# Kernel tuning notes

Measured on AMD Instinct MI355X. Metric: run time of the kernel, lower is better.

## Reference

```python
import jax, jax.numpy as jnp
import numpy as np
import math

NP_, NA_ = 100000, 50000          # paper / author node counts
E0, E1, E2 = 300000, 300000, 200000  # author->paper, paper->author, paper->paper
H, D = 4, 16
HID = H * D                       # 64
IN_DIM, OUT_DIM = 128, 64
L = 2                             # num_layers
EPS = 1e-5


def _lin(x, W, b):
    return x @ W + b


def _ln(x, g, b):
    m = jnp.mean(x, axis=-1, keepdims=True)
    v = jnp.mean((x - m) ** 2, axis=-1, keepdims=True)
    return (x - m) * jax.lax.rsqrt(v + EPS) * g + b


def _segment_softmax(a, seg, n):
    m = jax.ops.segment_max(a, seg, num_segments=n)
    a = jnp.exp(a - m[seg])
    s = jax.ops.segment_sum(a, seg, num_segments=n)
    return a / (s[seg] + 1e-16)


def _hgt_conv(h_p, h_a, ei_ap, ei_pa, ei_pp,
              W_kqv, b_kqv, W_krel, W_vrel, p_rel, W_hout, b_hout, skip):
    # per-node-type fused KQV projection (HeteroDictLinear)
    kqv_p = _lin(h_p, W_kqv[0], b_kqv[0])   # [NP, 3*HID]
    kqv_a = _lin(h_a, W_kqv[1], b_kqv[1])   # [NA, 3*HID]
    k_p, q_p, v_p = [t.reshape(-1, H, D) for t in jnp.split(kqv_p, 3, axis=1)]
    k_a, q_a, v_a = [t.reshape(-1, H, D) for t in jnp.split(kqv_a, 3, axis=1)]
    # destination (query) concat order: paper then author -> dst offsets {paper:0, author:NP}
    Q = jnp.concatenate([q_p, q_a], axis=0)                    # [NP+NA, H, D]
    # per-(edge_type, head) DxD relation transforms on source k/v (k_rel / v_rel)
    # src concat order follows edge types: et0 src=author, et1 src=paper, et2 src=paper
    Ks = jnp.concatenate([
        jnp.einsum('nhd,hde->nhe', k_a, W_krel[0]),
        jnp.einsum('nhd,hde->nhe', k_p, W_krel[1]),
        jnp.einsum('nhd,hde->nhe', k_p, W_krel[2]),
    ], axis=0)                                                 # [NA+2*NP, H, D]
    Vs = jnp.concatenate([
        jnp.einsum('nhd,hde->nhe', v_a, W_vrel[0]),
        jnp.einsum('nhd,hde->nhe', v_p, W_vrel[1]),
        jnp.einsum('nhd,hde->nhe', v_p, W_vrel[2]),
    ], axis=0)
    # bipartite global edge index (src offsets: 0, NA, NA+NP; dst offsets: paper 0, author NP)
    src = jnp.concatenate([ei_ap[0], ei_pa[0] + NA_, ei_pp[0] + NA_ + NP_])
    dst = jnp.concatenate([ei_ap[1], ei_pa[1] + NP_, ei_pp[1]])
    p = jnp.concatenate([
        jnp.broadcast_to(p_rel[0], (E0, H)),
        jnp.broadcast_to(p_rel[1], (E1, H)),
        jnp.broadcast_to(p_rel[2], (E2, H)),
    ], axis=0)                                                 # [E, H]
    # edge-wise attention: alpha = (q_i * k_j).sum(-1) * p_rel / sqrt(D), segment-softmax over dst
    alpha = jnp.einsum('ehd,ehd->eh', Q[dst], Ks[src]) * p / math.sqrt(D)
    alpha = _segment_softmax(alpha, dst, NP_ + NA_)
    out = jax.ops.segment_sum(Vs[src] * alpha[:, :, None], dst,
                              num_segments=NP_ + NA_)          # [NP+NA, H, D]
    out = out.reshape(-1, HID)
    g = jax.nn.gelu(out, approximate=False)
    o_p = _lin(g[:NP_], W_hout[0], b_hout[0])
    o_a = _lin(g[NP_:], W_hout[1], b_hout[1])
    a_p = jax.nn.sigmoid(skip[0])
    a_a = jax.nn.sigmoid(skip[1])
    return a_p * o_p + (1.0 - a_p) * h_p, a_a * o_a + (1.0 - a_a) * h_a


def _forward(x_paper, x_author, ei_ap, ei_pa, ei_pp,
             W_in, b_in, W_kqv, b_kqv, W_krel, W_vrel, p_rel,
             W_hout, b_hout, skip, ln_g, ln_b, W_out, b_out):
    h_p = _lin(x_paper, W_in[0], b_in[0])
    h_a = _lin(x_author, W_in[1], b_in[1])
    for l in range(L):
        h_p, h_a = _hgt_conv(h_p, h_a, ei_ap, ei_pa, ei_pp,
                             W_kqv[l], b_kqv[l], W_krel[l], W_vrel[l],
                             p_rel[l], W_hout[l], b_hout[l], skip[l])
        h_p = jax.nn.gelu(_ln(h_p, ln_g[l, 0], ln_b[l, 0]), approximate=False)
        h_a = jax.nn.gelu(_ln(h_a, ln_g[l, 1], ln_b[l, 1]), approximate=False)
        # dropout is identity at eval
    out_p = _lin(h_p, W_out[0], b_out[0])
    out_a = _lin(h_a, W_out[1], b_out[1])
    return jnp.concatenate([out_p, out_a], axis=0)  # [NP+NA, OUT_DIM]


def setup_inputs() -> dict:
    key = jax.random.key(0)
    ks = jax.random.split(key, 20)
    f32 = jnp.float32

    def nrm(k, shape, fan_in):
        return jax.random.normal(k, shape, dtype=f32) * (1.0 / math.sqrt(fan_in))

    inp = {}
    inp['x_paper'] = jax.random.normal(ks[0], (NP_, IN_DIM), dtype=f32)
    inp['x_author'] = jax.random.normal(ks[1], (NA_, IN_DIM), dtype=f32)
    inp['ei_ap'] = jnp.stack([jax.random.randint(ks[2], (E0,), 0, NA_),
                              jax.random.randint(ks[3], (E0,), 0, NP_)]).astype(jnp.int32)
    inp['ei_pa'] = jnp.stack([jax.random.randint(ks[4], (E1,), 0, NP_),
                              jax.random.randint(ks[5], (E1,), 0, NA_)]).astype(jnp.int32)
    inp['ei_pp'] = jnp.stack([jax.random.randint(ks[6], (E2,), 0, NP_),
                              jax.random.randint(ks[7], (E2,), 0, NP_)]).astype(jnp.int32)
    inp['W_in'] = nrm(ks[8], (2, IN_DIM, HID), IN_DIM)
    inp['b_in'] = jnp.zeros((2, HID), f32)
    inp['W_kqv'] = nrm(ks[9], (L, 2, HID, 3 * HID), HID)
    inp['b_kqv'] = jnp.zeros((L, 2, 3 * HID), f32)
    inp['W_krel'] = nrm(ks[10], (L, 3, H, D, D), D)
    inp['W_vrel'] = nrm(ks[11], (L, 3, H, D, D), D)
    inp['p_rel'] = jnp.ones((L, 3, H), f32)
    inp['W_hout'] = nrm(ks[12], (L, 2, HID, HID), HID)
    inp['b_hout'] = jnp.zeros((L, 2, HID), f32)
    inp['skip'] = jnp.ones((L, 2), f32)
    inp['ln_g'] = jnp.ones((L, 2, HID), f32)
    inp['ln_b'] = jnp.zeros((L, 2, HID), f32)
    inp['W_out'] = nrm(ks[13], (2, HID, OUT_DIM), HID)
    inp['b_out'] = jnp.zeros((2, OUT_DIM), f32)
    return inp


def reference(x_paper, x_author, ei_ap, ei_pa, ei_pp,
              W_in, b_in, W_kqv, b_kqv, W_krel, W_vrel, p_rel,
              W_hout, b_hout, skip, ln_g, ln_b, W_out, b_out):
    return _forward(x_paper, x_author, ei_ap, ei_pa, ei_pp,
                    W_in, b_in, W_kqv, b_kqv, W_krel, W_vrel, p_rel,
                    W_hout, b_hout, skip, ln_g, ln_b, W_out, b_out)
```

## Files before the change

### kernel.cpp

```cpp
#include <hip/hip_runtime.h>
#include <hip/hip_bf16.h>

#define NP 100000
#define NA 50000
#define NTOT 150000
#define E0 300000
#define E1 300000
#define E2 200000
#define ETOT 800000
#define NH 4
#define HD 16
#define HID 64
#define IN_DIM 128
#define KQV 192
#define LAYERS 2
#define NSRC 250000
#define JP 320
#define JA 192
#define NCH 586
#define PT 1563
#define AT 782

typedef __attribute__((ext_vector_type(8))) short bf16x8;
typedef __attribute__((ext_vector_type(4))) float f32x4;
typedef _Float16 h16x2 __attribute__((ext_vector_type(2)));

__device__ __forceinline__ float gelu_exact(float x) {
    return 0.5f * x * (1.0f + erff(x * 0.7071067811865475f));
}
__device__ __forceinline__ unsigned short f2bf(float f) {
    unsigned u = __float_as_uint(f);
    return (unsigned short)((u + 0x7fffu + ((u >> 16) & 1u)) >> 16);
}
__device__ __forceinline__ float bf2f(unsigned short b) {
    return __uint_as_float((unsigned)b << 16);
}
__device__ __forceinline__ unsigned short f2h(float f) {
    union { _Float16 h; unsigned short u; } c;
    c.h = (_Float16)f;
    return c.u;
}

__device__ __forceinline__ void edge_decode(int e, const int* __restrict__ ei_ap,
                                            const int* __restrict__ ei_pa,
                                            const int* __restrict__ ei_pp,
                                            int& src, int& dst) {
    if (e < E0)            { src = ei_ap[e];                 dst = ei_ap[E0 + e]; }
    else if (e < E0 + E1)  { int le = e - E0;
                             src = NA + ei_pa[le];           dst = NP + ei_pa[E1 + le]; }
    else                   { int le = e - E0 - E1;
                             src = NA + NP + ei_pp[le];      dst = ei_pp[E2 + le]; }
}

__global__ void zero_int_kernel(int* __restrict__ p, int n) {
    int i = blockIdx.x * blockDim.x + threadIdx.x;
    int st = gridDim.x * blockDim.x;
    for (int j = i; j < n; j += st) p[j] = 0;
}

__global__ void csr_count_kernel(const int* __restrict__ ei_ap, const int* __restrict__ ei_pa,
                                 const int* __restrict__ ei_pp, int* __restrict__ cnt) {
    int e = blockIdx.x * 256 + threadIdx.x;
    if (e >= ETOT) return;
    int src, dst; edge_decode(e, ei_ap, ei_pa, ei_pp, src, dst);
    atomicAdd(&cnt[dst], 1);
}

__global__ void scan_chunk_sums(const int* __restrict__ cnt, int* __restrict__ csum) {
    __shared__ int sd[256];
    int c = blockIdx.x, t = threadIdx.x;
    int i = c * 256 + t;
    sd[t] = (i < NTOT) ? cnt[i] : 0;
    __syncthreads();
    for (int o = 128; o > 0; o >>= 1) { if (t < o) sd[t] += sd[t + o]; __syncthreads(); }
    if (t == 0) csum[c] = sd[0];
}

__global__ void scan_offsets(const int* __restrict__ csum, int* __restrict__ coff, int nch) {
    __shared__ int sd[1024];
    int t = threadIdx.x;
    int v = (t < nch) ? csum[t] : 0;
    sd[t] = v;
    __syncthreads();
    for (int o = 1; o < 1024; o <<= 1) {
        int x = (t >= o) ? sd[t - o] : 0;
        __syncthreads();
        sd[t] += x;
        __syncthreads();
    }
    if (t < nch) coff[t] = sd[t] - v;
}

__global__ void scan_final(const int* __restrict__ cnt, const int* __restrict__ coff,
                           int* __restrict__ row_ptr, int* __restrict__ cursor) {
    __shared__ int sd[256];
    int c = blockIdx.x, t = threadIdx.x, i = c * 256 + t;
    int v = (i < NTOT) ? cnt[i] : 0;
    sd[t] = v;
    __syncthreads();
    for (int o = 1; o < 256; o <<= 1) {
        int x = (t >= o) ? sd[t - o] : 0;
        __syncthreads();
        sd[t] += x;
        __syncthreads();
    }
    if (i < NTOT) { int ex = coff[c] + sd[t] - v; row_ptr[i] = ex; cursor[i] = ex; }
    if (i == 0) row_ptr[NTOT] = ETOT;
}

__global__ void csr_fill_kernel(const int* __restrict__ ei_ap, const int* __restrict__ ei_pa,
                                const int* __restrict__ ei_pp, int* __restrict__ cursor,
                                int* __restrict__ edge_src) {
    int e = blockIdx.x * 256 + threadIdx.x;
    if (e >= ETOT) return;
    int src, dst; edge_decode(e, ei_ap, ei_pa, ei_pp, src, dst);
    int pos = atomicAdd(&cursor[dst], 1);
    edge_src[pos] = src;
}

__global__ void fuse_weights_kernel(const float* __restrict__ Wkqv, const float* __restrict__ bkqv,
                                    const float* __restrict__ Wkrel, const float* __restrict__ Wvrel,
                                    float* __restrict__ Wfp, float* __restrict__ bfp,
                                    float* __restrict__ Wfa, float* __restrict__ bfa) {
    int idx = blockIdx.x * 256 + threadIdx.x;
    int type, i, j;
    if (idx < 65 * JP) { type = 0; i = idx / JP; j = idx % JP; }
    else {
        int r = idx - 65 * JP;
        if (r >= 65 * JA) return;
        type = 1; i = r / JA; j = r % JA;
    }
    int c = j >> 6, jj = j & 63, h = jj >> 4, e = jj & 15;
    const float* Wk = Wkqv + (size_t)type * HID * KQV;
    const float* bk = bkqv + type * KQV;
    float val;
    if (c == 0) {
        val = (i < 64) ? Wk[i * KQV + 64 + jj] : bk[64 + jj];
    } else {
        int et, isV;
        if (type == 0) { et = (c == 1 || c == 3) ? 1 : 2; isV = (c >= 3); }
        else           { et = 0; isV = (c == 2); }
        const float* Wr = (isV ? Wvrel : Wkrel) + (size_t)(et * NH + h) * HD * HD;
        int sb = (isV ? 128 : 0) + h * HD;
        val = 0.0f;
        #pragma unroll
        for (int d = 0; d < HD; d++) {
            float a = (i < 64) ? Wk[i * KQV + sb + d] : bk[sb + d];
            val += a * Wr[d * HD + e];
        }
    }
    if (i < 64) (type ? Wfa : Wfp)[i * (type ? JA : JP) + j] = val;
    else        (type ? bfa : bfp)[j] = val;
}

__global__ __launch_bounds__(256) void gemm_in(
    const float* __restrict__ xp, const float* __restrict__ xa,
    const float* __restrict__ W_in, const float* __restrict__ b_in,
    unsigned short* __restrict__ Hb)
{
    __shared__ unsigned short Xb[64][136];
    __shared__ unsigned short Wt[64][136];
    int b = blockIdx.x, tid = threadIdx.x;
    int type = (b >= PT);
    int tile = type ? (b - PT) : b;
    int N = type ? NA : NP;
    const float* X = type ? xa : xp;
    const float* W = W_in + (size_t)type * IN_DIM * HID;
    const float* bias = b_in + type * HID;
    unsigned short* H = Hb + (type ? (size_t)NP * HID : 0);
    int nb = tile * 64;

    {
        int row = tid >> 2, c0 = (tid & 3) * 32;
        int n = nb + row;
        if (n < N) {
            const float* xr = X + (size_t)n * IN_DIM + c0;
            #pragma unroll
            for (int i = 0; i < 32; i += 4) {
                float4 v = *(const float4*)(xr + i);
                *(ushort4*)&Xb[row][c0 + i] =
                    make_ushort4(f2bf(v.x), f2bf(v.y), f2bf(v.z), f2bf(v.w));
            }
        } else {
            #pragma unroll
            for (int i = 0; i < 32; i += 4)
                *(ushort4*)&Xb[row][c0 + i] = make_ushort4(0, 0, 0, 0);
        }
    }
    #pragma unroll
    for (int it = 0; it < 8; it++) {
        int idx = it * 256 + tid;
        int k = idx & 127, c = (idx >> 7) * 4;
        float4 v = *(const float4*)(W + (size_t)k * HID + c);
        Wt[c + 0][k] = f2bf(v.x); Wt[c + 1][k] = f2bf(v.y);
        Wt[c + 2][k] = f2bf(v.z); Wt[c + 3][k] = f2bf(v.w);
    }
    __syncthreads();

    int w = tid >> 6, lane = tid & 63;
    int wr = (w >> 1) * 32, wc = (w & 1) * 32;
    int lrow = lane & 15, lgrp = lane >> 4;

    f32x4 acc00 = {0.f, 0.f, 0.f, 0.f};
    f32x4 acc01 = {0.f, 0.f, 0.f, 0.f};
    f32x4 acc10 = {0.f, 0.f, 0.f, 0.f};
    f32x4 acc11 = {0.f, 0.f, 0.f, 0.f};
    #pragma unroll
    for (int ks = 0; ks < 4; ks++) {
        int ko = ks * 32 + lgrp * 8;
        bf16x8 a0 = *(const bf16x8*)&Xb[wr + lrow][ko];
        bf16x8 a1 = *(const bf16x8*)&Xb[wr + 16 + lrow][ko];
        bf16x8 b0 = *(const bf16x8*)&Wt[wc + lrow][ko];
        bf16x8 b1 = *(const bf16x8*)&Wt[wc + 16 + lrow][ko];
        acc00 = __builtin_amdgcn_mfma_f32_16x16x32_bf16(a0, b0, acc00, 0, 0, 0);
        acc01 = __builtin_amdgcn_mfma_f32_16x16x32_bf16(a0, b1, acc01, 0, 0, 0);
        acc10 = __builtin_amdgcn_mfma_f32_16x16x32_bf16(a1, b0, acc10, 0, 0, 0);
        acc11 = __builtin_amdgcn_mfma_f32_16x16x32_bf16(a1, b1, acc11, 0, 0, 0);
    }

    float bias0 = bias[wc + lrow], bias1 = bias[wc + 16 + lrow];
    int c0 = wc + lrow, c1 = wc + 16 + lrow;
    bool even = ((lrow & 1) == 0);
    #pragma unroll
    for (int mi = 0; mi < 2; mi++) {
        const f32x4 accn0 = mi ? acc10 : acc00;
        const f32x4 accn1 = mi ? acc11 : acc01;
        int rbase = wr + mi * 16 + lgrp * 4;
        #pragma unroll
        for (int r = 0; r < 4; r++) {
            int n = nb + rbase + r;
            unsigned own = (unsigned)f2bf(accn0[r] + bias0)
                         | ((unsigned)f2bf(accn1[r] + bias1) << 16);
            unsigned oth = __shfl_xor(own, 1, 64);
            if (even && n < N) {
                unsigned* hp = (unsigned*)(H + (size_t)n * HID);
                hp[c0 >> 1] = (own & 0xffffu) | (oth << 16);
                hp[c1 >> 1] = (own >> 16) | (oth & 0xffff0000u);
            }
        }
    }
}

__global__ __launch_bounds__(256) void gemm_kqv(
    const unsigned short* __restrict__ Hb,
    const float* __restrict__ Wfp, const float* __restrict__ bfp,
    const float* __restrict__ Wfa, const float* __restrict__ bfa,
    unsigned short* __restrict__ Qh, unsigned* __restrict__ KVb)
{
    __shared__ unsigned short Xb[64][72];
    __shared__ unsigned short WtK[64][72];
    __shared__ unsigned short WtV[64][72];
    int b = blockIdx.x, tid = threadIdx.x;
    int type, tile, kind;
    if (b < PT)                { type = 0; kind = 0; tile = b; }
    else if (b < 2 * PT)       { type = 0; kind = 1; tile = b - PT; }
    else if (b < 3 * PT)       { type = 0; kind = 2; tile = b - 2 * PT; }
    else if (b < 3 * PT + AT)  { type = 1; kind = 0; tile = b - 3 * PT; }
    else                       { type = 1; kind = 1; tile = b - 3 * PT - AT; }
    int N = type ? NA : NP;
    const unsigned short* X = Hb + (type ? (size_t)NP * HID : 0);
    const float* W = type ? Wfa : Wfp;
    const float* bias = type ? bfa : bfp;
    int ldw = type ? JA : JP;
    int nb = tile * 64;
    bool isQ = (kind == 0);
    int kcol = 0, vcol = 0, noff = 0;
    if (!isQ) {
        if (type == 0) {
            if (kind == 1) { kcol = 64;  vcol = 192; noff = NA; }
            else           { kcol = 128; vcol = 256; noff = NA + NP; }
        } else             { kcol = 64;  vcol = 128; noff = 0; }
    } else {
        noff = type ? NP : 0;
    }

    {
        int row = tid >> 2, c0 = (tid & 3) * 16;
        int n = nb + row;
        if (n < N) {
            const unsigned short* xr = X + (size_t)n * HID + c0;
            *(ushort4*)&Xb[row][c0]      = *(const ushort4*)(xr);
            *(ushort4*)&Xb[row][c0 + 4]  = *(const ushort4*)(xr + 4);
            *(ushort4*)&Xb[row][c0 + 8]  = *(const ushort4*)(xr + 8);
            *(ushort4*)&Xb[row][c0 + 12] = *(const ushort4*)(xr + 12);
        } else {
            #pragma unroll
            for (int i = 0; i < 16; i += 4)
                *(ushort4*)&Xb[row][c0 + i] = make_ushort4(0, 0, 0, 0);
        }
    }
    #pragma unroll
    for (int it = 0; it < 4; it++) {
        int idx = it * 256 + tid;
        int k = idx & 63, c = (idx >> 6) * 4;
        float4 v = *(const float4*)(W + (size_t)k * ldw + kcol + c);
        WtK[c + 0][k] = f2bf(v.x); WtK[c + 1][k] = f2bf(v.y);
        WtK[c + 2][k] = f2bf(v.z); WtK[c + 3][k] = f2bf(v.w);
    }
    if (!isQ) {
        #pragma unroll
        for (int it = 0; it < 4; it++) {
            int idx = it * 256 + tid;
            int k = idx & 63, c = (idx >> 6) * 4;
            float4 v = *(const float4*)(W + (size_t)k * ldw + vcol + c);
            WtV[c + 0][k] = f2bf(v.x); WtV[c + 1][k] = f2bf(v.y);
            WtV[c + 2][k] = f2bf(v.z); WtV[c + 3][k] = f2bf(v.w);
        }
    }
    __syncthreads();

    int w = tid >> 6, lane = tid & 63;
    int wr = (w >> 1) * 32, wc = (w & 1) * 32;
    int lrow = lane & 15, lgrp = lane >> 4;

    f32x4 k00 = {0.f,0.f,0.f,0.f}, k01 = {0.f,0.f,0.f,0.f};
    f32x4 k10 = {0.f,0.f,0.f,0.f}, k11 = {0.f,0.f,0.f,0.f};
    f32x4 v00 = {0.f,0.f,0.f,0.f}, v01 = {0.f,0.f,0.f,0.f};
    f32x4 v10 = {0.f,0.f,0.f,0.f}, v11 = {0.f,0.f,0.f,0.f};
    #pragma unroll
    for (int ks = 0; ks < 2; ks++) {
        int ko = ks * 32 + lgrp * 8;
        bf16x8 a0 = *(const bf16x8*)&Xb[wr + lrow][ko];
        bf16x8 a1 = *(const bf16x8*)&Xb[wr + 16 + lrow][ko];
        bf16x8 bk0 = *(const bf16x8*)&WtK[wc + lrow][ko];
        bf16x8 bk1 = *(const bf16x8*)&WtK[wc + 16 + lrow][ko];
        k00 = __builtin_amdgcn_mfma_f32_16x16x32_bf16(a0, bk0, k00, 0, 0, 0);
        k01 = __builtin_amdgcn_mfma_f32_16x16x32_bf16(a0, bk1, k01, 0, 0, 0);
        k10 = __builtin_amdgcn_mfma_f32_16x16x32_bf16(a1, bk0, k10, 0, 0, 0);
        k11 = __builtin_amdgcn_mfma_f32_16x16x32_bf16(a1, bk1, k11, 0, 0, 0);
        if (!isQ) {
            bf16x8 bv0 = *(const bf16x8*)&WtV[wc + lrow][ko];
            bf16x8 bv1 = *(const bf16x8*)&WtV[wc + 16 + lrow][ko];
            v00 = __builtin_amdgcn_mfma_f32_16x16x32_bf16(a0, bv0, v00, 0, 0, 0);
            v01 = __builtin_amdgcn_mfma_f32_16x16x32_bf16(a0, bv1, v01, 0, 0, 0);
            v10 = __builtin_amdgcn_mfma_f32_16x16x32_bf16(a1, bv0, v10, 0, 0, 0);
            v11 = __builtin_amdgcn_mfma_f32_16x16x32_bf16(a1, bv1, v11, 0, 0, 0);
        }
    }

    int c0 = wc + lrow, c1 = wc + 16 + lrow;
    bool even = ((lrow & 1) == 0);
    if (isQ) {
        float bias0 = bias[c0], bias1 = bias[c1];
        #pragma unroll
        for (int mi = 0; mi < 2; mi++) {
            const f32x4 a0 = mi ? k10 : k00;
            const f32x4 a1 = mi ? k11 : k01;
            int rbase = wr + mi * 16 + lgrp * 4;
            #pragma unroll
            for (int r = 0; r < 4; r++) {
                int n = nb + rbase + r;
                unsigned own = (unsigned)f2h(a0[r] + bias0)
                             | ((unsigned)f2h(a1[r] + bias1) << 16);
                unsigned oth = __shfl_xor(own, 1, 64);
                if (even && n < N) {
                    unsigned* qp = (unsigned*)(Qh + (size_t)(noff + n) * HID);
                    qp[c0 >> 1] = (own & 0xffffu) | (oth << 16);
                    qp[c1 >> 1] = (own >> 16) | (oth & 0xffff0000u);
                }
            }
        }
    } else {
        float bk0 = bias[kcol + c0], bk1 = bias[kcol + c1];
        float bv0 = bias[vcol + c0], bv1 = bias[vcol + c1];
        #pragma unroll
        for (int mi = 0; mi < 2; mi++) {
            const f32x4 ak0 = mi ? k10 : k00;
            const f32x4 ak1 = mi ? k11 : k01;
            const f32x4 av0 = mi ? v10 : v00;
            const f32x4 av1 = mi ? v11 : v01;
            int rbase = wr + mi * 16 + lgrp * 4;
            #pragma unroll
            for (int r = 0; r < 4; r++) {
                int n = nb + rbase + r;
                unsigned* dst = KVb + (((size_t)(noff + n)) << 6);
                unsigned own0 = (unsigned)f2h(ak0[r] + bk0) | ((unsigned)f2h(av0[r] + bv0) << 16);
                unsigned oth0 = __shfl_xor(own0, 1, 64);
                unsigned own1 = (unsigned)f2h(ak1[r] + bk1) | ((unsigned)f2h(av1[r] + bv1) << 16);
                unsigned oth1 = __shfl_xor(own1, 1, 64);
                if (n < N) {
                    unsigned w0 = even ? ((own0 & 0xffffu) | (oth0 << 16))
                                       : ((oth0 >> 16) | (own0 & 0xffff0000u));
                    unsigned w1 = even ? ((own1 & 0xffffu) | (oth1 << 16))
                                       : ((oth1 >> 16) | (own1 & 0xffff0000u));
                    dst[c0] = w0;
                    dst[c1] = w1;
                }
            }
        }
    }
}

__global__ __launch_bounds__(256) void attn_kernel(
    const unsigned short* __restrict__ Qh, const unsigned* __restrict__ KVb,
    const float* __restrict__ p_rel, const int* __restrict__ row_ptr,
    const int* __restrict__ edge_src, unsigned short* __restrict__ ABf)
{
    int wid = threadIdx.x >> 6, lane = threadIdx.x & 63;
    int n = blockIdx.x * 4 + wid;
    if (n >= NTOT) return;
    int half = lane >> 5;
    int p = lane & 31;
    int h = p >> 3;
    unsigned qw = *(const unsigned*)(Qh + (((size_t)n) << 6) + 2 * p);
    union { unsigned u; h16x2 v; _Float16 f[2]; } qc; qc.u = qw;
    h16x2 qh = qc.v;
    const float INV_LN2 = 1.4426950408889634f;
    float pr0 = p_rel[h] * 0.25f * INV_LN2;
    float pr1 = p_rel[4 + h] * 0.25f * INV_LN2;
    float pr2 = p_rel[8 + h] * 0.25f * INV_LN2;
    int beg = row_ptr[n], end = row_ptr[n + 1];
    float s = 0.0f, acc0 = 0.f, acc1 = 0.f;
    for (int e = beg; e < end; e += 4) {
        int e0 = e + half;
        int e1 = e + 2 + half;
        bool v0 = (e0 < end), v1 = (e1 < end);
        int s0 = v0 ? edge_src[e0] : 0;
        int s1 = v1 ? edge_src[e1] : 0;
        uint2 kv0 = *(const uint2*)(KVb + (((size_t)s0) << 6) + 2 * p);
        uint2 kv1 = *(const uint2*)(KVb + (((size_t)s1) << 6) + 2 * p);
        float d0, d1;
#if __has_builtin(__builtin_amdgcn_fdot2)
        {
            union { unsigned u; h16x2 v; } ck;
            ck.u = kv0.x; d0 = __builtin_amdgcn_fdot2(qh, ck.v, 0.0f, false);
            ck.u = kv1.x; d1 = __builtin_amdgcn_fdot2(qh, ck.v, 0.0f, false);
        }
#else
        {
            union { unsigned u; _Float16 f[2]; } ck;
            float q0 = (float)qc.f[0], q1 = (float)qc.f[1];
            ck.u = kv0.x; d0 = q0 * (float)ck.f[0] + q1 * (float)ck.f[1];
            ck.u = kv1.x; d1 = q0 * (float)ck.f[0] + q1 * (float)ck.f[1];
        }
#endif
        d0 += __shfl_xor(d0, 1, 64);  d1 += __shfl_xor(d1, 1, 64);
        d0 += __shfl_xor(d0, 2, 64);  d1 += __shfl_xor(d1, 2, 64);
        d0 += __shfl_xor(d0, 4, 64);  d1 += __shfl_xor(d1, 4, 64);
        float pa = (s0 < NA) ? pr0 : ((s0 < NA + NP) ? pr1 : pr2);
        float pb = (s1 < NA) ? pr0 : ((s1 < NA + NP) ? pr1 : pr2);
        float a0 = v0 ? fminf(d0 * pa, 80.0f) : -INFINITY;
        float a1 = v1 ? fminf(d1 * pb, 80.0f) : -INFINITY;
        float p0 = exp2f(a0);
        float p1 = exp2f(a1);
        s += p0 + p1;
        union { unsigned u; _Float16 f[2]; } cv0, cv1;
        cv0.u = kv0.y; cv1.u = kv1.y;
        acc0 += p0 * (float)cv0.f[0] + p1 * (float)cv1.f[0];
        acc1 += p0 * (float)cv0.f[1] + p1 * (float)cv1.f[1];
    }
    s    += __shfl_xor(s, 32, 64);
    acc0 += __shfl_xor(acc0, 32, 64);
    acc1 += __shfl_xor(acc1, 32, 64);
    if (half == 0) {
        float inv = 1.0f / (s + 1e-16f);
        unsigned pack = (unsigned)f2bf(acc0 * inv) | ((unsigned)f2bf(acc1 * inv) << 16);
        *(unsigned*)(ABf + (((size_t)n) << 6) + 2 * p) = pack;
    }
}

__global__ __launch_bounds__(256) void gemm_hout(
    const unsigned short* __restrict__ ABf, const float* __restrict__ Whout,
    const float* __restrict__ bhout, const float* __restrict__ skip_p,
    const float* __restrict__ lng, const float* __restrict__ lnb,
    unsigned short* __restrict__ Hb,
    const float* __restrict__ Wout, const float* __restrict__ bout,
    float* __restrict__ outp)
{
    __shared__ unsigned short Xb[64][72];
    __shared__ unsigned short Wt[64][72];
    __shared__ float hs[64][68];
    int b = blockIdx.x, tid = threadIdx.x;
    int type = (b >= PT);
    int tile = type ? (b - PT) : b;
    int N = type ? NA : NP;
    size_t base_off = type ? (size_t)NP * HID : 0;
    const unsigned short* X = ABf + base_off;
    const float* W = Whout + (size_t)type * HID * HID;
    const float* bias = bhout + type * HID;
    unsigned short* H = Hb + base_off;
    int nb = tile * 64;
    bool fuse_out = (Wout != nullptr);

    {
        int row = tid >> 2, c0 = (tid & 3) * 16;
        int n = nb + row;
        unsigned short tmp[16];
        if (n < N) {
            const unsigned short* xr = X + (((size_t)n) << 6) + c0;
            #pragma unroll
            for (int i = 0; i < 16; i += 4) {
                ushort4 v = *(const ushort4*)(xr + i);
                tmp[i]   = f2bf(gelu_exact(bf2f(v.x)));
                tmp[i+1] = f2bf(gelu_exact(bf2f(v.y)));
                tmp[i+2] = f2bf(gelu_exact(bf2f(v.z)));
                tmp[i+3] = f2bf(gelu_exact(bf2f(v.w)));
            }
        } else {
            #pragma unroll
            for (int i = 0; i < 16; i++) tmp[i] = 0;
        }
        #pragma unroll
        for (int i = 0; i < 16; i += 4)
            *(ushort4*)&Xb[row][c0 + i] = make_ushort4(tmp[i], tmp[i+1], tmp[i+2], tmp[i+3]);
    }
    #pragma unroll
    for (int it = 0; it < 4; it++) {
        int idx = it * 256 + tid;
        int k = idx & 63, c = (idx >> 6) * 4;
        float4 v = *(const float4*)(W + (size_t)k * HID + c);
        Wt[c + 0][k] = f2bf(v.x); Wt[c + 1][k] = f2bf(v.y);
        Wt[c + 2][k] = f2bf(v.z); Wt[c + 3][k] = f2bf(v.w);
    }
    __syncthreads();

    int w = tid >> 6, lane = tid & 63;
    int wr = (w >> 1) * 32, wc = (w & 1) * 32;
    int lrow = lane & 15, lgrp = lane >> 4;

    f32x4 acc00 = {0.f, 0.f, 0.f, 0.f};
    f32x4 acc01 = {0.f, 0.f, 0.f, 0.f};
    f32x4 acc10 = {0.f, 0.f, 0.f, 0.f};
    f32x4 acc11 = {0.f, 0.f, 0.f, 0.f};
    #pragma unroll
    for (int ks = 0; ks < 2; ks++) {
        int ko = ks * 32 + lgrp * 8;
        bf16x8 a0 = *(const bf16x8*)&Xb[wr + lrow][ko];
        bf16x8 a1 = *(const bf16x8*)&Xb[wr + 16 + lrow][ko];
        bf16x8 b0 = *(const bf16x8*)&Wt[wc + lrow][ko];
        bf16x8 b1 = *(const bf16x8*)&Wt[wc + 16 + lrow][ko];
        acc00 = __builtin_amdgcn_mfma_f32_16x16x32_bf16(a0, b0, acc00, 0, 0, 0);
        acc01 = __builtin_amdgcn_mfma_f32_16x16x32_bf16(a0, b1, acc01, 0, 0, 0);
        acc10 = __builtin_amdgcn_mfma_f32_16x16x32_bf16(a1, b0, acc10, 0, 0, 0);
        acc11 = __builtin_amdgcn_mfma_f32_16x16x32_bf16(a1, b1, acc11, 0, 0, 0);
    }

    float a = 1.0f / (1.0f + __expf(-skip_p[type]));
    float oma = 1.0f - a;
    float bias0 = bias[wc + lrow], bias1 = bias[wc + 16 + lrow];
    #pragma unroll
    for (int mi = 0; mi < 2; mi++) {
        const f32x4 accn0 = mi ? acc10 : acc00;
        const f32x4 accn1 = mi ? acc11 : acc01;
        int rbase = wr + mi * 16 + lgrp * 4;
        #pragma unroll
        for (int r = 0; r < 4; r++) {
            int row = rbase + r;
            int n = nb + row;
            if (n < N) {
                const unsigned short* hp = H + (size_t)n * HID;
                hs[row][wc + lrow]      = a * (accn0[r] + bias0) + oma * bf2f(hp[wc + lrow]);
                hs[row][wc + 16 + lrow] = a * (accn1[r] + bias1) + oma * bf2f(hp[wc + 16 + lrow]);
            } else {
                hs[row][wc + lrow] = 0.f;
                hs[row][wc + 16 + lrow] = 0.f;
            }
        }
    }
    __syncthreads();

    const int tr = tid >> 4, tc = tid & 15;
    const int tcj = tc * 4;
    float g0 = lng[type*HID+tcj], g1 = lng[type*HID+tcj+1],
          g2 = lng[type*HID+tcj+2], g3 = lng[type*HID+tcj+3];
    float l0 = lnb[type*HID+tcj], l1 = lnb[type*HID+tcj+1],
          l2 = lnb[type*HID+tcj+2], l3 = lnb[type*HID+tcj+3];
    #pragma unroll 1
    for (int m = 0; m < 4; m++) {
        int row = tr * 4 + m;
        int n = nb + row;
        float v0 = hs[row][tcj], v1 = hs[row][tcj+1], v2 = hs[row][tcj+2], v3 = hs[row][tcj+3];
        float sum = v0 + v1 + v2 + v3;
        sum += __shfl_xor(sum, 1, 64); sum += __shfl_xor(sum, 2, 64);
        sum += __shfl_xor(sum, 4, 64); sum += __shfl_xor(sum, 8, 64);
        float mean = sum * (1.0f / 64.0f);
        float d0 = v0 - mean, d1 = v1 - mean, d2 = v2 - mean, d3 = v3 - mean;
        float sq = d0*d0 + d1*d1 + d2*d2 + d3*d3;
        sq += __shfl_xor(sq, 1, 64); sq += __shfl_xor(sq, 2, 64);
        sq += __shfl_xor(sq, 4, 64); sq += __shfl_xor(sq, 8, 64);
        float rstd = rsqrtf(sq * (1.0f / 64.0f) + 1e-5f);
        float r0 = gelu_exact(d0 * rstd * g0 + l0);
        float r1 = gelu_exact(d1 * rstd * g1 + l1);
        float r2 = gelu_exact(d2 * rstd * g2 + l2);
        float r3 = gelu_exact(d3 * rstd * g3 + l3);
        hs[row][tcj] = r0; hs[row][tcj+1] = r1;
        hs[row][tcj+2] = r2; hs[row][tcj+3] = r3;
        if (!fuse_out && n < N) {
            uint2 pk;
            pk.x = (unsigned)f2bf(r0) | ((unsigned)f2bf(r1) << 16);
            pk.y = (unsigned)f2bf(r2) | ((unsigned)f2bf(r3) << 16);
            *(uint2*)(H + (size_t)n * HID + tcj) = pk;
        }
    }

    if (fuse_out) {
        __syncthreads();
        {
            int row = tid >> 2, c0 = (tid & 3) * 16;
            #pragma unroll
            for (int i = 0; i < 16; i += 4) {
                *(ushort4*)&Xb[row][c0 + i] = make_ushort4(
                    f2bf(hs[row][c0 + i]),     f2bf(hs[row][c0 + i + 1]),
                    f2bf(hs[row][c0 + i + 2]), f2bf(hs[row][c0 + i + 3]));
            }
        }
        const float* W2 = Wout + (size_t)type * HID * HID;
        #pragma unroll
        for (int it = 0; it < 4; it++) {
            int idx = it * 256 + tid;
            int k = idx & 63, c = (idx >> 6) * 4;
            float4 v = *(const float4*)(W2 + (size_t)k * HID + c);
            Wt[c + 0][k] = f2bf(v.x); Wt[c + 1][k] = f2bf(v.y);
            Wt[c + 2][k] = f2bf(v.z); Wt[c + 3][k] = f2bf(v.w);
        }
        __syncthreads();

        f32x4 o00 = {0.f,0.f,0.f,0.f}, o01 = {0.f,0.f,0.f,0.f};
        f32x4 o10 = {0.f,0.f,0.f,0.f}, o11 = {0.f,0.f,0.f,0.f};
        #pragma unroll
        for (int ks = 0; ks < 2; ks++) {
            int ko = ks * 32 + lgrp * 8;
            bf16x8 a0 = *(const bf16x8*)&Xb[wr + lrow][ko];
            bf16x8 a1 = *(const bf16x8*)&Xb[wr + 16 + lrow][ko];
            bf16x8 b0 = *(const bf16x8*)&Wt[wc + lrow][ko];
            bf16x8 b1 = *(const bf16x8*)&Wt[wc + 16 + lrow][ko];
            o00 = __builtin_amdgcn_mfma_f32_16x16x32_bf16(a0, b0, o00, 0, 0, 0);
            o01 = __builtin_amdgcn_mfma_f32_16x16x32_bf16(a0, b1, o01, 0, 0, 0);
            o10 = __builtin_amdgcn_mfma_f32_16x16x32_bf16(a1, b0, o10, 0, 0, 0);
            o11 = __builtin_amdgcn_mfma_f32_16x16x32_bf16(a1, b1, o11, 0, 0, 0);
        }
        const float* b2 = bout + type * HID;
        float b20 = b2[wc + lrow], b21 = b2[wc + 16 + lrow];
        float* O = outp + base_off;
        #pragma unroll
        for (int mi = 0; mi < 2; mi++) {
            const f32x4 on0 = mi ? o10 : o00;
            const f32x4 on1 = mi ? o11 : o01;
            int rbase = wr + mi * 16 + lgrp * 4;
            #pragma unroll
            for (int r = 0; r < 4; r++) {
                int n = nb + rbase + r;
                if (n >= N) continue;
                O[(size_t)n * HID + wc + lrow]      = on0[r] + b20;
                O[(size_t)n * HID + wc + 16 + lrow] = on1[r] + b21;
            }
        }
    }
}

extern "C" void kernel_launch(void* const* d_in, const int* in_sizes, int n_in,
                              void* d_out, int out_size, void* d_ws, size_t ws_size,
                              hipStream_t stream) {
    const float* x_paper  = (const float*)d_in[0];
    const float* x_author = (const float*)d_in[1];
    const int*   ei_ap    = (const int*)d_in[2];
    const int*   ei_pa    = (const int*)d_in[3];
    const int*   ei_pp    = (const int*)d_in[4];
    const float* W_in     = (const float*)d_in[5];
    const float* b_in     = (const float*)d_in[6];
    const float* W_kqv    = (const float*)d_in[7];
    const float* b_kqv    = (const float*)d_in[8];
    const float* W_krel   = (const float*)d_in[9];
    const float* W_vrel   = (const float*)d_in[10];
    const float* p_rel    = (const float*)d_in[11];
    const float* W_hout   = (const float*)d_in[12];
    const float* b_hout   = (const float*)d_in[13];
    const float* skip     = (const float*)d_in[14];
    const float* ln_g     = (const float*)d_in[15];
    const float* ln_b     = (const float*)d_in[16];
    const float* W_out    = (const float*)d_in[17];
    const float* b_out    = (const float*)d_in[18];
    float* out            = (float*)d_out;

    char* ws = (char*)d_ws;
    unsigned short* Hb  = (unsigned short*)ws;
    unsigned short* Qh  = Hb + (size_t)NTOT * HID;
    unsigned* KVb       = (unsigned*)(Qh + (size_t)NTOT * HID);
    unsigned short* ABf = (unsigned short*)(KVb + (size_t)NSRC * HID);
    float* Wfp  = (float*)(ABf + (size_t)NTOT * HID);
    float* bfp  = Wfp  + 64 * JP;
    float* Wfa  = bfp  + JP;
    float* bfa  = Wfa  + 64 * JA;
    int* cnt      = (int*)(bfa + JA);
    int* row_ptr  = cnt + NTOT;
    int* cursor   = row_ptr + NTOT + 16;
    int* edge_src = cursor + NTOT;
    int* csum     = edge_src + ETOT;
    int* coff     = csum + 1024;

    dim3 blk(256);
    const int EB = (ETOT + 255) / 256;

    zero_int_kernel<<<256, blk, 0, stream>>>(cnt, NTOT);
    csr_count_kernel<<<EB, blk, 0, stream>>>(ei_ap, ei_pa, ei_pp, cnt);
    scan_chunk_sums<<<NCH, blk, 0, stream>>>(cnt, csum);
    scan_offsets<<<1, 1024, 0, stream>>>(csum, coff, NCH);
    scan_final<<<NCH, blk, 0, stream>>>(cnt, coff, row_ptr, cursor);
    csr_fill_kernel<<<EB, blk, 0, stream>>>(ei_ap, ei_pa, ei_pp, cursor, edge_src);

    gemm_in<<<PT + AT, blk, 0, stream>>>(x_paper, x_author, W_in, b_in, Hb);

    for (int l = 0; l < LAYERS; l++) {
        fuse_weights_kernel<<<(65 * JP + 65 * JA + 255) / 256, blk, 0, stream>>>(
            W_kqv + (size_t)l * 2 * HID * KQV, b_kqv + (size_t)l * 2 * KQV,
            W_krel + (size_t)l * 3 * NH * HD * HD, W_vrel + (size_t)l * 3 * NH * HD * HD,
            Wfp, bfp, Wfa, bfa);
        gemm_kqv<<<3 * PT + 2 * AT, blk, 0, stream>>>(
            Hb, Wfp, bfp, Wfa, bfa, Qh, KVb);
        attn_kernel<<<(NTOT + 3) / 4, blk, 0, stream>>>(
            Qh, KVb, p_rel + l * 3 * NH, row_ptr, edge_src, ABf);
        bool last = (l == LAYERS - 1);
        gemm_hout<<<PT + AT, blk, 0, stream>>>(
            ABf, W_hout + (size_t)l * 2 * HID * HID, b_hout + l * 2 * HID,
            skip + l * 2, ln_g + l * 2 * HID, ln_b + l * 2 * HID, Hb,
            last ? W_out : nullptr, last ? b_out : nullptr, last ? out : nullptr);
    }
}
```

Measured before the change: 390.3 us.

## Pretranspose weights to bf16 and merge Q into KV projection blocks

A new prep kernel converts W_in, W_hout and W_out once into transposed bf16 layouts, and fuse_weights now writes the fused KQV weights transposed in bf16. The GEMM kernels can then fill shared memory with vector copies instead of converting and scattering per element on every block. gemm_kqv also computes Q together with one K/V pair in the same block, which cuts the grid from 3*PT+2*AT to 2*PT+AT so each activation tile is loaded fewer times. The cost is extra shared memory and accumulator registers per block, plus one more launch.

```diff
diff --git a/kernel.cpp b/kernel.cpp
--- a/kernel.cpp
+++ b/kernel.cpp
@@ -118,10 +118,37 @@
     edge_src[pos] = src;
 }
 
+__global__ void prep_weights(const float* __restrict__ W_in, const float* __restrict__ W_hout,
+                             const float* __restrict__ W_out,
+                             unsigned short* __restrict__ WinT,
+                             unsigned short* __restrict__ WhoutT,
+                             unsigned short* __restrict__ WoutT) {
+    int idx = blockIdx.x * 256 + threadIdx.x;
+    if (idx < 2 * 64 * IN_DIM) {
+        int t = idx >> 13, r = idx & 8191;
+        int c = r >> 7, k = r & 127;
+        WinT[idx] = f2bf(W_in[(size_t)t * IN_DIM * HID + (size_t)k * HID + c]);
+        return;
+    }
+    int i2 = idx - 2 * 64 * IN_DIM;
+    if (i2 < LAYERS * 2 * 4096) {
+        int p = i2 >> 12, r = i2 & 4095;
+        int c = r >> 6, k = r & 63;
+        WhoutT[i2] = f2bf(W_hout[(size_t)p * 4096 + (size_t)k * HID + c]);
+        return;
+    }
+    int i3 = i2 - LAYERS * 2 * 4096;
+    if (i3 < 2 * 4096) {
+        int p = i3 >> 12, r = i3 & 4095;
+        int c = r >> 6, k = r & 63;
+        WoutT[i3] = f2bf(W_out[(size_t)p * 4096 + (size_t)k * HID + c]);
+    }
+}
+
 __global__ void fuse_weights_kernel(const float* __restrict__ Wkqv, const float* __restrict__ bkqv,
                                     const float* __restrict__ Wkrel, const float* __restrict__ Wvrel,
-                                    float* __restrict__ Wfp, float* __restrict__ bfp,
-                                    float* __restrict__ Wfa, float* __restrict__ bfa) {
+                                    unsigned short* __restrict__ WfpT, float* __restrict__ bfp,
+                                    unsigned short* __restrict__ WfaT, float* __restrict__ bfa) {
     int idx = blockIdx.x * 256 + threadIdx.x;
     int type, i, j;
     if (idx < 65 * JP) { type = 0; i = idx / JP; j = idx % JP; }
@@ -149,13 +176,13 @@
             val += a * Wr[d * HD + e];
         }
     }
-    if (i < 64) (type ? Wfa : Wfp)[i * (type ? JA : JP) + j] = val;
+    if (i < 64) (type ? WfaT : WfpT)[(size_t)j * 64 + i] = f2bf(val);
     else        (type ? bfa : bfp)[j] = val;
 }
 
 __global__ __launch_bounds__(256) void gemm_in(
     const float* __restrict__ xp, const float* __restrict__ xa,
-    const float* __restrict__ W_in, const float* __restrict__ b_in,
+    const unsigned short* __restrict__ WinT, const float* __restrict__ b_in,
     unsigned short* __restrict__ Hb)
 {
     __shared__ unsigned short Xb[64][136];
@@ -165,7 +192,7 @@
     int tile = type ? (b - PT) : b;
     int N = type ? NA : NP;
     const float* X = type ? xa : xp;
-    const float* W = W_in + (size_t)type * IN_DIM * HID;
+    const unsigned short* WT = WinT + (size_t)type * 64 * IN_DIM;
     const float* bias = b_in + type * HID;
     unsigned short* H = Hb + (type ? (size_t)NP * HID : 0);
     int nb = tile * 64;
@@ -190,10 +217,8 @@
     #pragma unroll
     for (int it = 0; it < 8; it++) {
         int idx = it * 256 + tid;
-        int k = idx & 127, c = (idx >> 7) * 4;
-        float4 v = *(const float4*)(W + (size_t)k * HID + c);
-        Wt[c + 0][k] = f2bf(v.x); Wt[c + 1][k] = f2bf(v.y);
-        Wt[c + 2][k] = f2bf(v.z); Wt[c + 3][k] = f2bf(v.w);
+        int c = idx >> 5, kg = (idx & 31) * 4;
+        *(ushort4*)&Wt[c][kg] = *(const ushort4*)(WT + (size_t)c * IN_DIM + kg);
     }
     __syncthreads();
 
@@ -243,36 +268,30 @@
 
 __global__ __launch_bounds__(256) void gemm_kqv(
     const unsigned short* __restrict__ Hb,
-    const float* __restrict__ Wfp, const float* __restrict__ bfp,
-    const float* __restrict__ Wfa, const float* __restrict__ bfa,
+    const unsigned short* __restrict__ WfpT, const float* __restrict__ bfp,
+    const unsigned short* __restrict__ WfaT, const float* __restrict__ bfa,
     unsigned short* __restrict__ Qh, unsigned* __restrict__ KVb)
 {
     __shared__ unsigned short Xb[64][72];
+    __shared__ unsigned short WtQ[64][72];
     __shared__ unsigned short WtK[64][72];
     __shared__ unsigned short WtV[64][72];
     int b = blockIdx.x, tid = threadIdx.x;
-    int type, tile, kind;
-    if (b < PT)                { type = 0; kind = 0; tile = b; }
-    else if (b < 2 * PT)       { type = 0; kind = 1; tile = b - PT; }
-    else if (b < 3 * PT)       { type = 0; kind = 2; tile = b - 2 * PT; }
-    else if (b < 3 * PT + AT)  { type = 1; kind = 0; tile = b - 3 * PT; }
-    else                       { type = 1; kind = 1; tile = b - 3 * PT - AT; }
+    int type, tile;
+    bool hasQ;
+    int kcol, vcol, noff;
+    if (b < PT)        { type = 0; tile = b;          hasQ = true;
+                         kcol = 64;  vcol = 192; noff = NA; }
+    else if (b < 2*PT) { type = 0; tile = b - PT;     hasQ = false;
+                         kcol = 128; vcol = 256; noff = NA + NP; }
+    else               { type = 1; tile = b - 2*PT;   hasQ = true;
+                         kcol = 64;  vcol = 128; noff = 0; }
     int N = type ? NA : NP;
     const unsigned short* X = Hb + (type ? (size_t)NP * HID : 0);
-    const float* W = type ? Wfa : Wfp;
+    const unsigned short* WT = type ? WfaT : WfpT;
     const float* bias = type ? bfa : bfp;
-    int ldw = type ? JA : JP;
     int nb = tile * 64;
-    bool isQ = (kind == 0);
-    int kcol = 0, vcol = 0, noff = 0;
-    if (!isQ) {
-        if (type == 0) {
-            if (kind == 1) { kcol = 64;  vcol = 192; noff = NA; }
-            else           { kcol = 128; vcol = 256; noff = NA + NP; }
-        } else             { kcol = 64;  vcol = 128; noff = 0; }
-    } else {
-        noff = type ? NP : 0;
-    }
+    int qnoff = type ? NP : 0;
 
     {
         int row = tid >> 2, c0 = (tid & 3) * 16;
@@ -292,20 +311,11 @@
     #pragma unroll
     for (int it = 0; it < 4; it++) {
         int idx = it * 256 + tid;
-        int k = idx & 63, c = (idx >> 6) * 4;
-        float4 v = *(const float4*)(W + (size_t)k * ldw + kcol + c);
-        WtK[c + 0][k] = f2bf(v.x); WtK[c + 1][k] = f2bf(v.y);
-        WtK[c + 2][k] = f2bf(v.z); WtK[c + 3][k] = f2bf(v.w);
-    }
-    if (!isQ) {
-        #pragma unroll
-        for (int it = 0; it < 4; it++) {
-            int idx = it * 256 + tid;
-            int k = idx & 63, c = (idx >> 6) * 4;
-            float4 v = *(const float4*)(W + (size_t)k * ldw + vcol + c);
-            WtV[c + 0][k] = f2bf(v.x); WtV[c + 1][k] = f2bf(v.y);
-            WtV[c + 2][k] = f2bf(v.z); WtV[c + 3][k] = f2bf(v.w);
-        }
+        int c = idx >> 4, kg = (idx & 15) * 4;
+        *(ushort4*)&WtK[c][kg] = *(const ushort4*)(WT + (size_t)(kcol + c) * 64 + kg);
+        *(ushort4*)&WtV[c][kg] = *(const ushort4*)(WT + (size_t)(vcol + c) * 64 + kg);
+        if (hasQ)
+            *(ushort4*)&WtQ[c][kg] = *(const ushort4*)(WT + (size_t)c * 64 + kg);
     }
     __syncthreads();
 
@@ -313,6 +323,8 @@
     int wr = (w >> 1) * 32, wc = (w & 1) * 32;
     int lrow = lane & 15, lgrp = lane >> 4;
 
+    f32x4 q00 = {0.f,0.f,0.f,0.f}, q01 = {0.f,0.f,0.f,0.f};
+    f32x4 q10 = {0.f,0.f,0.f,0.f}, q11 = {0.f,0.f,0.f,0.f};
     f32x4 k00 = {0.f,0.f,0.f,0.f}, k01 = {0.f,0.f,0.f,0.f};
     f32x4 k10 = {0.f,0.f,0.f,0.f}, k11 = {0.f,0.f,0.f,0.f};
     f32x4 v00 = {0.f,0.f,0.f,0.f}, v01 = {0.f,0.f,0.f,0.f};
@@ -328,39 +340,46 @@
         k01 = __builtin_amdgcn_mfma_f32_16x16x32_bf16(a0, bk1, k01, 0, 0, 0);
         k10 = __builtin_amdgcn_mfma_f32_16x16x32_bf16(a1, bk0, k10, 0, 0, 0);
         k11 = __builtin_amdgcn_mfma_f32_16x16x32_bf16(a1, bk1, k11, 0, 0, 0);
-        if (!isQ) {
-            bf16x8 bv0 = *(const bf16x8*)&WtV[wc + lrow][ko];
-            bf16x8 bv1 = *(const bf16x8*)&WtV[wc + 16 + lrow][ko];
-            v00 = __builtin_amdgcn_mfma_f32_16x16x32_bf16(a0, bv0, v00, 0, 0, 0);
-            v01 = __builtin_amdgcn_mfma_f32_16x16x32_bf16(a0, bv1, v01, 0, 0, 0);
-            v10 = __builtin_amdgcn_mfma_f32_16x16x32_bf16(a1, bv0, v10, 0, 0, 0);
-            v11 = __builtin_amdgcn_mfma_f32_16x16x32_bf16(a1, bv1, v11, 0, 0, 0);
+        bf16x8 bv0 = *(const bf16x8*)&WtV[wc + lrow][ko];
+        bf16x8 bv1 = *(const bf16x8*)&WtV[wc + 16 + lrow][ko];
+        v00 = __builtin_amdgcn_mfma_f32_16x16x32_bf16(a0, bv0, v00, 0, 0, 0);
+        v01 = __builtin_amdgcn_mfma_f32_16x16x32_bf16(a0, bv1, v01, 0, 0, 0);
+        v10 = __builtin_amdgcn_mfma_f32_16x16x32_bf16(a1, bv0, v10, 0, 0, 0);
+        v11 = __builtin_amdgcn_mfma_f32_16x16x32_bf16(a1, bv1, v11, 0, 0, 0);
+        if (hasQ) {
+            bf16x8 bq0 = *(const bf16x8*)&WtQ[wc + lrow][ko];
+            bf16x8 bq1 = *(const bf16x8*)&WtQ[wc + 16 + lrow][ko];
+            q00 = __builtin_amdgcn_mfma_f32_16x16x32_bf16(a0, bq0, q00, 0, 0, 0);
+            q01 = __builtin_amdgcn_mfma_f32_16x16x32_bf16(a0, bq1, q01, 0, 0, 0);
+            q10 = __builtin_amdgcn_mfma_f32_16x16x32_bf16(a1, bq0, q10, 0, 0, 0);
+            q11 = __builtin_amdgcn_mfma_f32_16x16x32_bf16(a1, bq1, q11, 0, 0, 0);
         }
     }
 
     int c0 = wc + lrow, c1 = wc + 16 + lrow;
     bool even = ((lrow & 1) == 0);
-    if (isQ) {
-        float bias0 = bias[c0], bias1 = bias[c1];
+    if (hasQ) {
+        float bq0 = bias[c0], bq1 = bias[c1];
         #pragma unroll
         for (int mi = 0; mi < 2; mi++) {
-            const f32x4 a0 = mi ? k10 : k00;
-            const f32x4 a1 = mi ? k11 : k01;
+            const f32x4 a0 = mi ? q10 : q00;
+            const f32x4 a1 = mi ? q11 : q01;
             int rbase = wr + mi * 16 + lgrp * 4;
             #pragma unroll
             for (int r = 0; r < 4; r++) {
                 int n = nb + rbase + r;
-                unsigned own = (unsigned)f2h(a0[r] + bias0)
-                             | ((unsigned)f2h(a1[r] + bias1) << 16);
+                unsigned own = (unsigned)f2h(a0[r] + bq0)
+                             | ((unsigned)f2h(a1[r] + bq1) << 16);
                 unsigned oth = __shfl_xor(own, 1, 64);
                 if (even && n < N) {
-                    unsigned* qp = (unsigned*)(Qh + (size_t)(noff + n) * HID);
+                    unsigned* qp = (unsigned*)(Qh + (size_t)(qnoff + n) * HID);
                     qp[c0 >> 1] = (own & 0xffffu) | (oth << 16);
                     qp[c1 >> 1] = (own >> 16) | (oth & 0xffff0000u);
                 }
             }
         }
-    } else {
+    }
+    {
         float bk0 = bias[kcol + c0], bk1 = bias[kcol + c1];
         float bv0 = bias[vcol + c0], bv1 = bias[vcol + c1];
         #pragma unroll
@@ -460,11 +479,11 @@
 }
 
 __global__ __launch_bounds__(256) void gemm_hout(
-    const unsigned short* __restrict__ ABf, const float* __restrict__ Whout,
+    const unsigned short* __restrict__ ABf, const unsigned short* __restrict__ WhT,
     const float* __restrict__ bhout, const float* __restrict__ skip_p,
     const float* __restrict__ lng, const float* __restrict__ lnb,
     unsigned short* __restrict__ Hb,
-    const float* __restrict__ Wout, const float* __restrict__ bout,
+    const unsigned short* __restrict__ WoT, const float* __restrict__ bout,
     float* __restrict__ outp)
 {
     __shared__ unsigned short Xb[64][72];
@@ -476,11 +495,11 @@
     int N = type ? NA : NP;
     size_t base_off = type ? (size_t)NP * HID : 0;
     const unsigned short* X = ABf + base_off;
-    const float* W = Whout + (size_t)type * HID * HID;
+    const unsigned short* W = WhT + (size_t)type * 4096;
     const float* bias = bhout + type * HID;
     unsigned short* H = Hb + base_off;
     int nb = tile * 64;
-    bool fuse_out = (Wout != nullptr);
+    bool fuse_out = (WoT != nullptr);
 
     {
         int row = tid >> 2, c0 = (tid & 3) * 16;
@@ -507,10 +526,8 @@
     #pragma unroll
     for (int it = 0; it < 4; it++) {
         int idx = it * 256 + tid;
-        int k = idx & 63, c = (idx >> 6) * 4;
-        float4 v = *(const float4*)(W + (size_t)k * HID + c);
-        Wt[c + 0][k] = f2bf(v.x); Wt[c + 1][k] = f2bf(v.y);
-        Wt[c + 2][k] = f2bf(v.z); Wt[c + 3][k] = f2bf(v.w);
+        int c = idx >> 4, kg = (idx & 15) * 4;
+        *(ushort4*)&Wt[c][kg] = *(const ushort4*)(W + (size_t)c * 64 + kg);
     }
     __syncthreads();
 
@@ -604,14 +621,12 @@
                     f2bf(hs[row][c0 + i + 2]), f2bf(hs[row][c0 + i + 3]));
             }
         }
-        const float* W2 = Wout + (size_t)type * HID * HID;
+        const unsigned short* W2 = WoT + (size_t)type * 4096;
         #pragma unroll
         for (int it = 0; it < 4; it++) {
             int idx = it * 256 + tid;
-            int k = idx & 63, c = (idx >> 6) * 4;
-            float4 v = *(const float4*)(W2 + (size_t)k * HID + c);
-            Wt[c + 0][k] = f2bf(v.x); Wt[c + 1][k] = f2bf(v.y);
-            Wt[c + 2][k] = f2bf(v.z); Wt[c + 3][k] = f2bf(v.w);
+            int c = idx >> 4, kg = (idx & 15) * 4;
+            *(ushort4*)&Wt[c][kg] = *(const ushort4*)(W2 + (size_t)c * 64 + kg);
         }
         __syncthreads();
 
@@ -677,11 +692,14 @@
     unsigned short* Qh  = Hb + (size_t)NTOT * HID;
     unsigned* KVb       = (unsigned*)(Qh + (size_t)NTOT * HID);
     unsigned short* ABf = (unsigned short*)(KVb + (size_t)NSRC * HID);
-    float* Wfp  = (float*)(ABf + (size_t)NTOT * HID);
-    float* bfp  = Wfp  + 64 * JP;
-    float* Wfa  = bfp  + JP;
-    float* bfa  = Wfa  + 64 * JA;
-    int* cnt      = (int*)(bfa + JA);
+    unsigned short* WfpT = ABf + (size_t)NTOT * HID;
+    float* bfp  = (float*)(WfpT + (size_t)JP * 64);
+    unsigned short* WfaT = (unsigned short*)(bfp + JP);
+    float* bfa  = (float*)(WfaT + (size_t)JA * 64);
+    unsigned short* WinT   = (unsigned short*)(bfa + JA);
+    unsigned short* WhoutT = WinT + 2 * 64 * IN_DIM;
+    unsigned short* WoutT  = WhoutT + LAYERS * 2 * 64 * 64;
+    int* cnt      = (int*)(WoutT + 2 * 64 * 64);
     int* row_ptr  = cnt + NTOT;
     int* cursor   = row_ptr + NTOT + 16;
     int* edge_src = cursor + NTOT;
@@ -698,21 +716,24 @@
     scan_final<<<NCH, blk, 0, stream>>>(cnt, coff, row_ptr, cursor);
     csr_fill_kernel<<<EB, blk, 0, stream>>>(ei_ap, ei_pa, ei_pp, cursor, edge_src);
 
-    gemm_in<<<PT + AT, blk, 0, stream>>>(x_paper, x_author, W_in, b_in, Hb);
+    prep_weights<<<(2*64*IN_DIM + LAYERS*2*4096 + 2*4096 + 255) / 256, blk, 0, stream>>>(
+        W_in, W_hout, W_out, WinT, WhoutT, WoutT);
+
+    gemm_in<<<PT + AT, blk, 0, stream>>>(x_paper, x_author, WinT, b_in, Hb);
 
     for (int l = 0; l < LAYERS; l++) {
         fuse_weights_kernel<<<(65 * JP + 65 * JA + 255) / 256, blk, 0, stream>>>(
             W_kqv + (size_t)l * 2 * HID * KQV, b_kqv + (size_t)l * 2 * KQV,
             W_krel + (size_t)l * 3 * NH * HD * HD, W_vrel + (size_t)l * 3 * NH * HD * HD,
-            Wfp, bfp, Wfa, bfa);
-        gemm_kqv<<<3 * PT + 2 * AT, blk, 0, stream>>>(
-            Hb, Wfp, bfp, Wfa, bfa, Qh, KVb);
+            WfpT, bfp, WfaT, bfa);
+        gemm_kqv<<<2 * PT + AT, blk, 0, stream>>>(
+            Hb, WfpT, bfp, WfaT, bfa, Qh, KVb);
         attn_kernel<<<(NTOT + 3) / 4, blk, 0, stream>>>(
             Qh, KVb, p_rel + l * 3 * NH, row_ptr, edge_src, ABf);
         bool last = (l == LAYERS - 1);
         gemm_hout<<<PT + AT, blk, 0, stream>>>(
-            ABf, W_hout + (size_t)l * 2 * HID * HID, b_hout + l * 2 * HID,
+            ABf, WhoutT + (size_t)l * 2 * 4096, b_hout + l * 2 * HID,
             skip + l * 2, ln_g + l * 2 * HID, ln_b + l * 2 * HID, Hb,
-            last ? W_out : nullptr, last ? b_out : nullptr, last ? out : nullptr);
-    }
-}
+            last ? WoutT : nullptr, last ? b_out : nullptr, last ? out : nullptr);
+    }
+}
```

Result: faster. 365.4 us (-6.4%).
